# Kernel tuning notes

Hardware: AMD Instinct MI355X
Metric: run time of the kernel (lower is better)

Reference implementation:

```python
import jax, jax.numpy as jnp
import numpy as np

Q = 3  # q_order: SelfONN concatenates powers x^1..x^Q on channel dim

def selfonn_conv(x, w, b, pad):
    # x: (B, C, H, W); w: (O, C*Q, kh, kw); b: (O,)
    xp = jnp.concatenate([x ** (i + 1) for i in range(Q)], axis=1)
    y = jax.lax.conv_general_dilated(
        xp, w, window_strides=(1, 1), padding=[(pad, pad), (pad, pad)],
        dimension_numbers=("NCHW", "OIHW", "NCHW"))
    return y + b[None, :, None, None]

def setup_inputs() -> dict:
    key = jax.random.key(0)
    ks = jax.random.split(key, 9)
    B, C, H, W = 4, 64, 64, 64
    P = 64  # pab_channels
    s1 = 1.0 / np.sqrt(C * Q)          # 1x1 convs
    s3 = 1.0 / np.sqrt(C * Q * 9)      # 3x3 convs
    return {
        "x": jax.random.normal(ks[0], (B, C, H, W), jnp.float32),
        "top_w": jax.random.normal(ks[1], (P, C * Q, 1, 1), jnp.float32) * s1,
        "top_b": jnp.zeros((P,), jnp.float32),
        "center_w": jax.random.normal(ks[2], (P, C * Q, 1, 1), jnp.float32) * s1,
        "center_b": jnp.zeros((P,), jnp.float32),
        "bottom_w": jax.random.normal(ks[3], (C, C * Q, 3, 3), jnp.float32) * s3,
        "bottom_b": jnp.zeros((C,), jnp.float32),
        "out_w": jax.random.normal(ks[4], (C, C * Q, 3, 3), jnp.float32) * s3,
        "out_b": jnp.zeros((C,), jnp.float32),
    }

def reference(x, top_w, top_b, center_w, center_b, bottom_w, bottom_b, out_w, out_b):
    B, C, H, W = x.shape
    HW = H * W
    x_top = selfonn_conv(x, top_w, top_b, 0).reshape(B, -1, HW)            # (B, P, HW)
    x_center = selfonn_conv(x, center_w, center_b, 0).reshape(B, -1, HW)  # (B, P, HW)
    x_bottom = selfonn_conv(x, bottom_w, bottom_b, 1).reshape(B, C, HW)   # (B, C, HW)
    x_center = jnp.swapaxes(x_center, 1, 2)  # (B, HW, P)
    x_bottom = jnp.swapaxes(x_bottom, 1, 2)  # (B, HW, C)
    sp = jnp.einsum("bnp,bpm->bnm", x_center, x_top)  # (B, HW, HW)
    # GLOBAL softmax over the entire HW*HW map per sample (dim=1 on flattened view)
    sp = jax.nn.softmax(sp.reshape(B, -1), axis=1).reshape(B, HW, HW)
    sp = jnp.einsum("bnm,bmc->bnc", sp, x_bottom)  # (B, HW, C)
    # faithful to torch: raw reshape (B, HW, C) -> (B, C, H, W), no transpose
    sp = sp.reshape(B, C, H, W)
    return selfonn_conv(x + sp, out_w, out_b, 1)
```

## Files before the change

kernel.cpp:

```cpp
#include <hip/hip_runtime.h>
#include <hip/hip_bf16.h>

namespace {
constexpr int IMG    = 262144;
constexpr int PADIMG = 4356;
constexpr float LOG2E = 1.44269504088896340736f;
constexpr int WBFO  = 0;
constexpr int XPADO = 122880;
constexpr int TOPO  = 1795584;
constexpr int CENO  = 2319872;
constexpr int BOTO  = 2844160;
constexpr int PVO   = 3368448;
constexpr int MSO4  = 5465600;
constexpr int MSO8  = 7562752;
constexpr size_t NEED8 = (size_t)(MSO8 + 8192) * 4;
}

using half8v  = __attribute__((ext_vector_type(8))) _Float16;
using half4v  = __attribute__((ext_vector_type(4))) _Float16;
using short8v = __attribute__((ext_vector_type(8))) short;
typedef __attribute__((ext_vector_type(4))) float f32x4;

__device__ __forceinline__ short f2bf(float f) {
    __hip_bfloat16 h = __float2bfloat16(f);
    return *reinterpret_cast<short*>(&h);
}
__device__ __forceinline__ float bf2f(short s) {
    unsigned u = ((unsigned)(unsigned short)s) << 16;
    return __uint_as_float(u);
}

__global__ __launch_bounds__(256) void k_prep(const float* __restrict__ bw, const float* __restrict__ ow,
                                              const float* __restrict__ tw, const float* __restrict__ cw,
                                              _Float16* __restrict__ wbf,
                                              const float* __restrict__ x, _Float16* __restrict__ xpad) {
    __shared__ float xs[64 * 65];
    int bx = blockIdx.x, t = threadIdx.x;
    if (bx < 960) {
        int idx = bx * 256 + t;
        if (idx < 221184) {
            int tsel = idx / 110592;
            int r    = idx - tsel * 110592;
            int tap  = r / 12288;
            int rr   = r - tap * 12288;
            int ck   = rr / 2048;
            int r2   = rr - ck * 2048;
            int o    = r2 >> 5;
            int ki   = r2 & 31;
            int k    = ck * 32 + ki;
            int p    = k >> 6, ci = k & 63;
            const float* src = tsel ? ow : bw;
            wbf[idx] = (_Float16)src[o * 1728 + (p * 64 + ci) * 9 + tap];
        } else {
            int j = idx - 221184;
            int tsel = j / 12288;
            int rr   = j - tsel * 12288;
            int ck   = rr / 2048;
            int r2   = rr - ck * 2048;
            int o    = r2 >> 5;
            int ki   = r2 & 31;
            int k    = ck * 32 + ki;
            wbf[idx] = (_Float16)(tsel ? cw[o * 192 + k] * LOG2E : tw[o * 192 + k]);
        }
        return;
    }
    int bx2 = bx - 960;
    int b = bx2 >> 6, h = bx2 & 63;
    {
        _Float16* base = xpad + (size_t)b * 6 * PADIMG * 32;
        int px[6];
        px[0] = (h + 1) * 66;
        px[1] = (h + 1) * 66 + 65;
        px[2] = h;
        px[3] = 65 * 66 + h;
        int npx = 4;
        if (h < 2) { px[4] = 64 + h; px[5] = 65 * 66 + 64 + h; npx = 6; }
        int pi = t / 24, ck = t % 24;
        if (pi < npx) {
            int cp = ck >> 2, q = ck & 3;
            half8v z = {0, 0, 0, 0, 0, 0, 0, 0};
            *(half8v*)&base[((size_t)cp * PADIMG + px[pi]) * 32 + q * 8] = z;
        }
    }
    #pragma unroll
    for (int it = 0; it < 16; ++it) {
        int idx = it * 256 + t;
        int ci = idx >> 6, wc = idx & 63;
        xs[ci * 65 + wc] = x[b * IMG + ci * 4096 + h * 64 + wc];
    }
    __syncthreads();
    _Float16* dst = xpad + ((size_t)b * 6 * PADIMG + (h + 1) * 66 + 1) * 32;
    #pragma unroll
    for (int it = 0; it < 6; ++it) {
        int u = it * 256 + t;
        int ck = u >> 8, within = u & 255;
        int px = within >> 2, q = within & 3;
        int k0 = ck * 32 + q * 8;
        int p = k0 >> 6, c0 = k0 & 63;
        half8v o;
        #pragma unroll
        for (int j = 0; j < 8; ++j) {
            float v = xs[(c0 + j) * 65 + px];
            float pw = (p == 0) ? v : ((p == 1) ? v * v : v * v * v);
            o[j] = (_Float16)pw;
        }
        *(half8v*)&dst[((size_t)ck * PADIMG + px) * 32 + q * 8] = o;
    }
}

__device__ __forceinline__ void conv3d32(int bx, int t,
                                         const _Float16* __restrict__ src,
                                         const _Float16* __restrict__ wt,
                                         const float* __restrict__ bias,
                                         _Float16* __restrict__ dh_, float* __restrict__ df) {
    int lane = t & 63, w = t >> 6;
    int l16 = lane & 15, quad = lane >> 4;
    int oh = bx >> 8, mt = bx & 255;
    int b = mt >> 6, h = mt & 63;
    const _Float16* abase = src + ((size_t)b * 6 * PADIMG + (h + 1) * 66 + 1 + w * 16 + l16) * 32 + quad * 8;
    const _Float16* bbase = wt + (size_t)(oh * 32 + l16) * 32 + quad * 8;
    f32x4 acc[2];
    acc[0] = (f32x4){0.f, 0.f, 0.f, 0.f};
    acc[1] = (f32x4){0.f, 0.f, 0.f, 0.f};
    for (int tap = 0; tap < 9; ++tap) {
        int dh = tap / 3 - 1, dw = tap % 3 - 1;
        const _Float16* arow = abase + (dh * 66 + dw) * 32;
        const _Float16* brow = bbase + (size_t)tap * 6 * 2048;
        #pragma unroll
        for (int c6 = 0; c6 < 6; ++c6) {
            half8v afr  = *(const half8v*)&arow[(size_t)c6 * PADIMG * 32];
            half8v bfr0 = *(const half8v*)&brow[(size_t)c6 * 2048];
            half8v bfr1 = *(const half8v*)&brow[(size_t)c6 * 2048 + 512];
            acc[0] = __builtin_amdgcn_mfma_f32_16x16x32_f16(afr, bfr0, acc[0], 0, 0, 0);
            acc[1] = __builtin_amdgcn_mfma_f32_16x16x32_f16(afr, bfr1, acc[1], 0, 0, 0);
        }
    }
    #pragma unroll
    for (int nf = 0; nf < 2; ++nf) {
        int c = oh * 32 + nf * 16 + l16;
        float bv = bias[c];
        size_t oi = (size_t)b * 262144 + (size_t)c * 4096 + h * 64 + w * 16 + quad * 4;
        if (dh_) {
            half4v o;
            #pragma unroll
            for (int r = 0; r < 4; ++r) o[r] = (_Float16)(acc[nf][r] + bv);
            *(half4v*)&dh_[oi] = o;
        } else {
            float4 o = make_float4(acc[nf][0] + bv, acc[nf][1] + bv, acc[nf][2] + bv, acc[nf][3] + bv);
            *(float4*)&df[oi] = o;
        }
    }
}

__global__ __launch_bounds__(256) void k_convs(const _Float16* __restrict__ xpad,
                                               const _Float16* __restrict__ wbf,
                                               const float* __restrict__ tb, const float* __restrict__ cb,
                                               const float* __restrict__ bbias,
                                               _Float16* __restrict__ topd, _Float16* __restrict__ cend,
                                               _Float16* __restrict__ botb) {
    int bx = blockIdx.x, t = threadIdx.x;
    if (bx < 512) {
        conv3d32(bx, t, xpad, wbf , bbias, botb, nullptr);
        return;
    }
    int bx2 = bx - 512;
    int lane = t & 63, w = t >> 6;
    int l16 = lane & 15, quad = lane >> 4;
    int ot = bx2 >> 8, mt = bx2 & 255;
    int b = mt >> 6, h = mt & 63;
    const _Float16* wt   = wbf + (ot ? 233472 : 221184);
    const float*    bias = ot ? cb : tb;
    _Float16*       dst  = (ot ? cend : topd) + (size_t)b * IMG;
    const _Float16* abase = xpad + ((size_t)b * 6 * PADIMG + (h + 1) * 66 + 1 + w * 16 + l16) * 32 + quad * 8;
    const _Float16* bbase = wt + (size_t)l16 * 32 + quad * 8;
    f32x4 acc[4];
    #pragma unroll
    for (int nf = 0; nf < 4; ++nf) acc[nf] = (f32x4){0.f, 0.f, 0.f, 0.f};
    #pragma unroll
    for (int kc = 0; kc < 6; ++kc) {
        half8v afr = *(const half8v*)&abase[(size_t)kc * PADIMG * 32];
        #pragma unroll
        for (int nf = 0; nf < 4; ++nf) {
            half8v bfr = *(const half8v*)&bbase[(size_t)kc * 2048 + nf * 16 * 32];
            acc[nf] = __builtin_amdgcn_mfma_f32_16x16x32_f16(afr, bfr, acc[nf], 0, 0, 0);
        }
    }
    _Float16* dp = dst + (size_t)(h * 64 + w * 16) * 64;
    #pragma unroll
    for (int nf = 0; nf < 4; ++nf) {
        float bv = bias[nf * 16 + l16];
        if (ot) bv *= LOG2E;
        #pragma unroll
        for (int r = 0; r < 4; ++r)
            dp[(quad * 4 + r) * 64 + nf * 16 + l16] = (_Float16)(acc[nf][r] + bv);
    }
}

__global__ __launch_bounds__(256) void k_attn(float* __restrict__ ws, int mtiles, int msoOff, int zsoOff) {
    __shared__ _Float16 ltop[64 * 72];
    __shared__ _Float16 lbot[64 * 72];
    __shared__ _Float16 lp[128 * 72];
    int t    = threadIdx.x;
    int lane = t & 63, w = t >> 6;
    int l16  = lane & 15, quad = lane >> 4;
    int bxr = blockIdx.x;
    int bx  = (bxr & 7) * ((int)gridDim.x >> 3) + (bxr >> 3);
    int st = bx & 31, b = (bx >> 5) & 3, s = bx >> 7;
    int n0 = st * 128;
    int mbase = s * mtiles * 64;
    const _Float16* topg = (const _Float16*)(ws + TOPO) + (size_t)b * IMG;
    const _Float16* ceng = (const _Float16*)(ws + CENO) + (size_t)b * IMG;
    const _Float16* botg = (const _Float16*)(ws + BOTO) + (size_t)b * IMG;

    half8v afr[2][2];
    #pragma unroll
    for (int i = 0; i < 2; ++i)
        #pragma unroll
        for (int kk = 0; kk < 2; ++kk)
            afr[i][kk] = *(const half8v*)&ceng[(size_t)(n0 + w * 32 + i * 16 + l16) * 64 + kk * 32 + quad * 8];

    int r0 = t >> 3, r1 = r0 + 32, off = (t & 7) * 8;
    int q2 = quad >> 1;
    int lpw = (w * 32 + quad * 4) * 72;
    int lpr = (w * 32 + l16) * 72;
    int rb3 = (l16 >> 3) & 1;

    f32x4 pv[2][4];
    #pragma unroll
    for (int i = 0; i < 2; ++i)
        #pragma unroll
        for (int j = 0; j < 4; ++j) pv[i][j] = (f32x4){0.f, 0.f, 0.f, 0.f};
    float runm = -3.0e38f, zacc = 0.f;

    half8v rt0 = *(const half8v*)&topg[(size_t)(mbase + r0) * 64 + off];
    half8v rt1 = *(const half8v*)&topg[(size_t)(mbase + r1) * 64 + off];
    half8v rb0 = *(const half8v*)&botg[(size_t)r0 * 4096 + mbase + off];
    half8v rb1 = *(const half8v*)&botg[(size_t)r1 * 4096 + mbase + off];

    for (int tt = 0; tt < mtiles; ++tt) {
        __syncthreads();
        *(half8v*)&ltop[r0 * 72 + off] = rt0;
        *(half8v*)&ltop[r1 * 72 + off] = rt1;
        *(half8v*)&lbot[r0 * 72 + off] = rb0;
        *(half8v*)&lbot[r1 * 72 + off] = rb1;
        __syncthreads();
        if (tt < mtiles - 1) {
            int m1 = mbase + (tt + 1) * 64;
            rt0 = *(const half8v*)&topg[(size_t)(m1 + r0) * 64 + off];
            rt1 = *(const half8v*)&topg[(size_t)(m1 + r1) * 64 + off];
            rb0 = *(const half8v*)&botg[(size_t)r0 * 4096 + m1 + off];
            rb1 = *(const half8v*)&botg[(size_t)r1 * 4096 + m1 + off];
        }
        f32x4 sa[2][4];
        #pragma unroll
        for (int i = 0; i < 2; ++i)
            #pragma unroll
            for (int j = 0; j < 4; ++j) sa[i][j] = (f32x4){0.f, 0.f, 0.f, 0.f};
        __builtin_amdgcn_s_setprio(1);
        #pragma unroll
        for (int kk = 0; kk < 2; ++kk)
            #pragma unroll
            for (int j = 0; j < 4; ++j) {
                half8v bfr = *(half8v*)&ltop[(j * 16 + l16) * 72 + kk * 32 + quad * 8];
                sa[0][j] = __builtin_amdgcn_mfma_f32_16x16x32_f16(afr[0][kk], bfr, sa[0][j], 0, 0, 0);
                sa[1][j] = __builtin_amdgcn_mfma_f32_16x16x32_f16(afr[1][kk], bfr, sa[1][j], 0, 0, 0);
            }
        __builtin_amdgcn_s_setprio(0);
        float tm = -3.0e38f;
        #pragma unroll
        for (int i = 0; i < 2; ++i)
            #pragma unroll
            for (int j = 0; j < 4; ++j) {
                float a = fmaxf(sa[i][j][0], sa[i][j][1]);
                float c = fmaxf(sa[i][j][2], sa[i][j][3]);
                tm = fmaxf(tm, fmaxf(a, c));
            }
        for (int o2 = 32; o2; o2 >>= 1) tm = fmaxf(tm, __shfl_xor(tm, o2, 64));
        float newm = fmaxf(runm, tm);
        if (newm > runm) {
            float sc = __builtin_amdgcn_exp2f(runm - newm);
            zacc *= sc;
            #pragma unroll
            for (int i = 0; i < 2; ++i)
                #pragma unroll
                for (int j = 0; j < 4; ++j) pv[i][j] *= sc;
            runm = newm;
        }
        #pragma unroll
        for (int i = 0; i < 2; ++i)
            #pragma unroll
            for (int j = 0; j < 4; ++j) {
                int cb = (j ^ q2) * 16 + l16;
                #pragma unroll
                for (int r = 0; r < 4; ++r) {
                    float e = __builtin_amdgcn_exp2f(sa[i][j][r] - runm);
                    zacc += e;
                    lp[lpw + i * 1152 + r * 72 + cb] = (_Float16)e;
                }
            }
        half8v pa[2][2];
        #pragma unroll
        for (int i = 0; i < 2; ++i)
            #pragma unroll
            for (int kk = 0; kk < 2; ++kk) {
                int jj = kk * 2 + q2;
                pa[i][kk] = *(half8v*)&lp[lpr + i * 1152 + ((jj ^ rb3) * 16) + (quad & 1) * 8];
            }
        __builtin_amdgcn_s_setprio(1);
        #pragma unroll
        for (int kk = 0; kk < 2; ++kk)
            #pragma unroll
            for (int j = 0; j < 4; ++j) {
                half8v bb = *(half8v*)&lbot[(j * 16 + l16) * 72 + kk * 32 + quad * 8];
                pv[0][j] = __builtin_amdgcn_mfma_f32_16x16x32_f16(pa[0][kk], bb, pv[0][j], 0, 0, 0);
                pv[1][j] = __builtin_amdgcn_mfma_f32_16x16x32_f16(pa[1][kk], bb, pv[1][j], 0, 0, 0);
            }
        __builtin_amdgcn_s_setprio(0);
    }
    for (int o2 = 32; o2; o2 >>= 1) zacc += __shfl_xor(zacc, o2, 64);
    if (lane == 0) {
        ws[msoOff + s * 512 + b * 128 + st * 4 + w] = runm;
        ws[zsoOff + s * 512 + b * 128 + st * 4 + w] = zacc;
    }
    short* pvp = (short*)(ws + PVO) + (size_t)s * 1048576 + (size_t)b * IMG;
    #pragma unroll
    for (int i = 0; i < 2; ++i)
        #pragma unroll
        for (int j = 0; j < 4; ++j)
            #pragma unroll
            for (int r = 0; r < 4; ++r)
                pvp[(size_t)(n0 + w * 32 + i * 16 + quad * 4 + r) * 64 + j * 16 + l16] = f2bf(pv[i][j][r]);
}

__global__ __launch_bounds__(512) void k_finalu(const float* __restrict__ x, float* __restrict__ ws,
                                                _Float16* __restrict__ upad,
                                                int ms, int msoOff, int zsoOff) {
    __shared__ float us[64 * 65];
    __shared__ float rm[8], rz[8];
    int t = threadIdx.x, bx = blockIdx.x;
    int b = bx >> 6, h = bx & 63;
    int g = t & 127;
    float m = -3.0e38f;
    for (int s = 0; s < ms; ++s)
        m = fmaxf(m, ws[msoOff + s * 512 + b * 128 + g]);
    for (int o2 = 32; o2; o2 >>= 1) m = fmaxf(m, __shfl_xor(m, o2, 64));
    if ((t & 63) == 0) rm[t >> 6] = m;
    __syncthreads();
    float M = rm[0];
    #pragma unroll
    for (int j = 1; j < 8; ++j) M = fmaxf(M, rm[j]);
    float z = 0.f;
    if (t < 128) {
        for (int s = 0; s < ms; ++s)
            z += ws[zsoOff + s * 512 + b * 128 + g] *
                 __builtin_amdgcn_exp2f(ws[msoOff + s * 512 + b * 128 + g] - M);
    }
    for (int o2 = 32; o2; o2 >>= 1) z += __shfl_xor(z, o2, 64);
    if ((t & 63) == 0) rz[t >> 6] = z;
    __syncthreads();
    float Z = 0.f;
    #pragma unroll
    for (int j = 0; j < 8; ++j) Z += rz[j];
    float rZ = 1.0f / Z;

    const short* pvb = (const short*)(ws + PVO) + (size_t)b * IMG;
    int hg = h >> 5;
    {
        int idx = t * 8;
        int ci = idx >> 6, wc = idx & 63;
        int rem = ci * 4096 + h * 64 + wc;
        int grp = ci * 2 + hg;
        float acc[8] = {};
        for (int s = 0; s < ms; ++s) {
            float scl = __builtin_amdgcn_exp2f(ws[msoOff + s * 512 + b * 128 + grp] - M);
            short8v pvv = *(const short8v*)&pvb[(size_t)s * 1048576 + rem];
            #pragma unroll
            for (int i = 0; i < 8; ++i) acc[i] += bf2f(pvv[i]) * scl;
        }
        float4 x0 = *(const float4*)&x[(size_t)b * IMG + rem];
        float4 x1 = *(const float4*)&x[(size_t)b * IMG + rem + 4];
        float xv[8] = {x0.x, x0.y, x0.z, x0.w, x1.x, x1.y, x1.z, x1.w};
        #pragma unroll
        for (int i = 0; i < 8; ++i)
            us[ci * 65 + wc + i] = xv[i] + acc[i] * rZ;
    }
    __syncthreads();
    _Float16* dst = upad + ((size_t)b * 6 * PADIMG + (h + 1) * 66 + 1) * 32;
    #pragma unroll
    for (int it = 0; it < 3; ++it) {
        int u = it * 512 + t;
        int ck = u >> 8, within = u & 255;
        int px = within >> 2, q = within & 3;
        int k0 = ck * 32 + q * 8;
        int p = k0 >> 6, c0 = k0 & 63;
        half8v o;
        #pragma unroll
        for (int j = 0; j < 8; ++j) {
            float v = us[(c0 + j) * 65 + px];
            float pw = (p == 0) ? v : ((p == 1) ? v * v : v * v * v);
            o[j] = (_Float16)pw;
        }
        *(half8v*)&dst[((size_t)ck * PADIMG + px) * 32 + q * 8] = o;
    }
}

__global__ __launch_bounds__(256) void k_conv3o(const _Float16* __restrict__ upad,
                                                const _Float16* __restrict__ wout,
                                                const float* __restrict__ ob,
                                                float* __restrict__ out) {
    conv3d32(blockIdx.x, threadIdx.x, upad, wout, ob, nullptr, out);
}

extern "C" void kernel_launch(void* const* d_in, const int* in_sizes, int n_in,
                              void* d_out, int out_size, void* d_ws, size_t ws_size,
                              hipStream_t stream) {
    (void)in_sizes; (void)n_in; (void)out_size;
    const float* x  = (const float*)d_in[0];
    const float* tw = (const float*)d_in[1];
    const float* tb = (const float*)d_in[2];
    const float* cw = (const float*)d_in[3];
    const float* cb = (const float*)d_in[4];
    const float* bw = (const float*)d_in[5];
    const float* bb = (const float*)d_in[6];
    const float* ow = (const float*)d_in[7];
    const float* ob = (const float*)d_in[8];
    float* ws  = (float*)d_ws;
    float* out = (float*)d_out;

    _Float16* wbf  = (_Float16*)(ws + WBFO);
    _Float16* wout = wbf + 110592;
    _Float16* xpad = (_Float16*)(ws + XPADO);
    _Float16* topb = (_Float16*)(ws + TOPO);
    _Float16* cenb = (_Float16*)(ws + CENO);
    _Float16* botb = (_Float16*)(ws + BOTO);

    int ms     = (ws_size >= NEED8) ? 8 : 4;
    int mtiles = 64 / ms;
    int msoOff = (ms == 8) ? MSO8 : MSO4;
    int zsoOff = msoOff + ms * 512;

    hipLaunchKernelGGL(k_prep, dim3(1216), dim3(256), 0, stream, bw, ow, tw, cw, wbf, x, xpad);
    hipLaunchKernelGGL(k_convs, dim3(1024), dim3(256), 0, stream, xpad, wbf, tb, cb, bb, topb, cenb, botb);
    hipLaunchKernelGGL(k_attn, dim3(128 * ms), dim3(256), 0, stream, ws, mtiles, msoOff, zsoOff);
    hipLaunchKernelGGL(k_finalu, dim3(256), dim3(512), 0, stream, x, ws, xpad, ms, msoOff, zsoOff);
    hipLaunchKernelGGL(k_conv3o, dim3(512), dim3(256), 0, stream, xpad, wout, ob, out);
}
```

Measured before the change: 168.7 us.

## Keep softmax probabilities in registers via transposed MFMA and lane permutes

Swaps the operand order of the score and PV MFMAs so results come out transposed. The exponentiated probabilities can then be repacked into f16 A/B fragments with cvt_pkrtz, v_permlane32_swap and ds_swizzle instead of a round trip through the LDS buffer. The LDS buffer is removed. Rescaling of the running max is deferred until the local max exceeds it by more than 8, which avoids a per-tile wave reduction. Output stores become 4-wide vectors. The changes add cross-lane permute instructions, and the lazy rescaling lets intermediate values grow up to 2^8, which risks f16 range or precision issues.

New measurement: 167.7 us. No clear change (-0.6%).

```diff
diff --git a/kernel.cpp b/kernel.cpp
--- a/kernel.cpp
+++ b/kernel.cpp
@@ -19,6 +19,8 @@
 using half8v  = __attribute__((ext_vector_type(8))) _Float16;
 using half4v  = __attribute__((ext_vector_type(4))) _Float16;
 using short8v = __attribute__((ext_vector_type(8))) short;
+using short4v = __attribute__((ext_vector_type(4))) short;
+using uint4v  = __attribute__((ext_vector_type(4))) unsigned;
 typedef __attribute__((ext_vector_type(4))) float f32x4;
 
 __device__ __forceinline__ short f2bf(float f) {
@@ -28,6 +30,9 @@
 __device__ __forceinline__ float bf2f(short s) {
     unsigned u = ((unsigned)(unsigned short)s) << 16;
     return __uint_as_float(u);
+}
+__device__ __forceinline__ unsigned pkrtz(float a, float b) {
+    return __builtin_bit_cast(unsigned, __builtin_amdgcn_cvt_pkrtz(a, b));
 }
 
 __global__ __launch_bounds__(256) void k_prep(const float* __restrict__ bw, const float* __restrict__ ow,
@@ -199,10 +204,10 @@
 __global__ __launch_bounds__(256) void k_attn(float* __restrict__ ws, int mtiles, int msoOff, int zsoOff) {
     __shared__ _Float16 ltop[64 * 72];
     __shared__ _Float16 lbot[64 * 72];
-    __shared__ _Float16 lp[128 * 72];
     int t    = threadIdx.x;
     int lane = t & 63, w = t >> 6;
     int l16  = lane & 15, quad = lane >> 4;
+    bool hi16 = (lane & 16) != 0;
     int bxr = blockIdx.x;
     int bx  = (bxr & 7) * ((int)gridDim.x >> 3) + (bxr >> 3);
     int st = bx & 31, b = (bx >> 5) & 3, s = bx >> 7;
@@ -212,24 +217,20 @@
     const _Float16* ceng = (const _Float16*)(ws + CENO) + (size_t)b * IMG;
     const _Float16* botg = (const _Float16*)(ws + BOTO) + (size_t)b * IMG;
 
-    half8v afr[2][2];
-    #pragma unroll
-    for (int i = 0; i < 2; ++i)
+    half8v bcen[2][2];
+    #pragma unroll
+    for (int nj = 0; nj < 2; ++nj)
         #pragma unroll
         for (int kk = 0; kk < 2; ++kk)
-            afr[i][kk] = *(const half8v*)&ceng[(size_t)(n0 + w * 32 + i * 16 + l16) * 64 + kk * 32 + quad * 8];
+            bcen[nj][kk] = *(const half8v*)&ceng[(size_t)(n0 + w * 32 + nj * 16 + l16) * 64 + kk * 32 + quad * 8];
 
     int r0 = t >> 3, r1 = r0 + 32, off = (t & 7) * 8;
-    int q2 = quad >> 1;
-    int lpw = (w * 32 + quad * 4) * 72;
-    int lpr = (w * 32 + l16) * 72;
-    int rb3 = (l16 >> 3) & 1;
-
-    f32x4 pv[2][4];
-    #pragma unroll
-    for (int i = 0; i < 2; ++i)
-        #pragma unroll
-        for (int j = 0; j < 4; ++j) pv[i][j] = (f32x4){0.f, 0.f, 0.f, 0.f};
+
+    f32x4 pv[4][2];
+    #pragma unroll
+    for (int cj = 0; cj < 4; ++cj)
+        #pragma unroll
+        for (int nj = 0; nj < 2; ++nj) pv[cj][nj] = (f32x4){0.f, 0.f, 0.f, 0.f};
     float runm = -3.0e38f, zacc = 0.f;
 
     half8v rt0 = *(const half8v*)&topg[(size_t)(mbase + r0) * 64 + off];
@@ -251,71 +252,85 @@
             rb0 = *(const half8v*)&botg[(size_t)r0 * 4096 + m1 + off];
             rb1 = *(const half8v*)&botg[(size_t)r1 * 4096 + m1 + off];
         }
-        f32x4 sa[2][4];
-        #pragma unroll
-        for (int i = 0; i < 2; ++i)
-            #pragma unroll
-            for (int j = 0; j < 4; ++j) sa[i][j] = (f32x4){0.f, 0.f, 0.f, 0.f};
+        f32x4 sa[4][2];
+        #pragma unroll
+        for (int mi = 0; mi < 4; ++mi)
+            #pragma unroll
+            for (int nj = 0; nj < 2; ++nj) sa[mi][nj] = (f32x4){0.f, 0.f, 0.f, 0.f};
         __builtin_amdgcn_s_setprio(1);
         #pragma unroll
         for (int kk = 0; kk < 2; ++kk)
             #pragma unroll
-            for (int j = 0; j < 4; ++j) {
-                half8v bfr = *(half8v*)&ltop[(j * 16 + l16) * 72 + kk * 32 + quad * 8];
-                sa[0][j] = __builtin_amdgcn_mfma_f32_16x16x32_f16(afr[0][kk], bfr, sa[0][j], 0, 0, 0);
-                sa[1][j] = __builtin_amdgcn_mfma_f32_16x16x32_f16(afr[1][kk], bfr, sa[1][j], 0, 0, 0);
+            for (int mi = 0; mi < 4; ++mi) {
+                half8v at = *(half8v*)&ltop[(mi * 16 + l16) * 72 + kk * 32 + quad * 8];
+                sa[mi][0] = __builtin_amdgcn_mfma_f32_16x16x32_f16(at, bcen[0][kk], sa[mi][0], 0, 0, 0);
+                sa[mi][1] = __builtin_amdgcn_mfma_f32_16x16x32_f16(at, bcen[1][kk], sa[mi][1], 0, 0, 0);
             }
         __builtin_amdgcn_s_setprio(0);
-        float tm = -3.0e38f;
-        #pragma unroll
-        for (int i = 0; i < 2; ++i)
-            #pragma unroll
-            for (int j = 0; j < 4; ++j) {
-                float a = fmaxf(sa[i][j][0], sa[i][j][1]);
-                float c = fmaxf(sa[i][j][2], sa[i][j][3]);
-                tm = fmaxf(tm, fmaxf(a, c));
-            }
-        for (int o2 = 32; o2; o2 >>= 1) tm = fmaxf(tm, __shfl_xor(tm, o2, 64));
-        float newm = fmaxf(runm, tm);
-        if (newm > runm) {
-            float sc = __builtin_amdgcn_exp2f(runm - newm);
-            zacc *= sc;
-            #pragma unroll
-            for (int i = 0; i < 2; ++i)
+        float lm = -3.0e38f;
+        #pragma unroll
+        for (int mi = 0; mi < 4; ++mi)
+            #pragma unroll
+            for (int nj = 0; nj < 2; ++nj) {
+                float a = fmaxf(sa[mi][nj][0], sa[mi][nj][1]);
+                float c2 = fmaxf(sa[mi][nj][2], sa[mi][nj][3]);
+                lm = fmaxf(lm, fmaxf(a, c2));
+            }
+        if (!__all(lm - runm <= 8.0f)) {
+            float tm = lm;
+            for (int o2 = 32; o2; o2 >>= 1) tm = fmaxf(tm, __shfl_xor(tm, o2, 64));
+            if (tm > runm) {
+                float sc = __builtin_amdgcn_exp2f(runm - tm);
+                zacc *= sc;
                 #pragma unroll
-                for (int j = 0; j < 4; ++j) pv[i][j] *= sc;
-            runm = newm;
-        }
-        #pragma unroll
-        for (int i = 0; i < 2; ++i)
-            #pragma unroll
-            for (int j = 0; j < 4; ++j) {
-                int cb = (j ^ q2) * 16 + l16;
+                for (int cj = 0; cj < 4; ++cj)
+                    #pragma unroll
+                    for (int nj = 0; nj < 2; ++nj) pv[cj][nj] *= sc;
+                runm = tm;
+            }
+        }
+        #pragma unroll
+        for (int kb = 0; kb < 2; ++kb) {
+            unsigned pk[2][2][2];
+            #pragma unroll
+            for (int f = 0; f < 2; ++f) {
+                int mi = 2 * kb + f;
                 #pragma unroll
-                for (int r = 0; r < 4; ++r) {
-                    float e = __builtin_amdgcn_exp2f(sa[i][j][r] - runm);
-                    zacc += e;
-                    lp[lpw + i * 1152 + r * 72 + cb] = (_Float16)e;
+                for (int nj = 0; nj < 2; ++nj) {
+                    float e0 = __builtin_amdgcn_exp2f(sa[mi][nj][0] - runm);
+                    float e1 = __builtin_amdgcn_exp2f(sa[mi][nj][1] - runm);
+                    float e2 = __builtin_amdgcn_exp2f(sa[mi][nj][2] - runm);
+                    float e3 = __builtin_amdgcn_exp2f(sa[mi][nj][3] - runm);
+                    zacc += (e0 + e1) + (e2 + e3);
+                    pk[f][nj][0] = pkrtz(e0, e1);
+                    pk[f][nj][1] = pkrtz(e2, e3);
                 }
             }
-        half8v pa[2][2];
-        #pragma unroll
-        for (int i = 0; i < 2; ++i)
-            #pragma unroll
-            for (int kk = 0; kk < 2; ++kk) {
-                int jj = kk * 2 + q2;
-                pa[i][kk] = *(half8v*)&lp[lpr + i * 1152 + ((jj ^ rb3) * 16) + (quad & 1) * 8];
-            }
-        __builtin_amdgcn_s_setprio(1);
-        #pragma unroll
-        for (int kk = 0; kk < 2; ++kk)
-            #pragma unroll
-            for (int j = 0; j < 4; ++j) {
-                half8v bb = *(half8v*)&lbot[(j * 16 + l16) * 72 + kk * 32 + quad * 8];
-                pv[0][j] = __builtin_amdgcn_mfma_f32_16x16x32_f16(pa[0][kk], bb, pv[0][j], 0, 0, 0);
-                pv[1][j] = __builtin_amdgcn_mfma_f32_16x16x32_f16(pa[1][kk], bb, pv[1][j], 0, 0, 0);
-            }
-        __builtin_amdgcn_s_setprio(0);
+            half8v pa[2];
+            #pragma unroll
+            for (int nj = 0; nj < 2; ++nj) {
+                unsigned T[4];
+                #pragma unroll
+                for (int d = 0; d < 2; ++d) {
+                    unsigned X = pk[0][nj][d], Y = pk[1][nj][d];
+                    asm("v_permlane32_swap_b32 %0, %1" : "+v"(X), "+v"(Y));
+                    unsigned A0s = __builtin_amdgcn_ds_swizzle(X, 0x401F);
+                    unsigned A1s = __builtin_amdgcn_ds_swizzle(Y, 0x401F);
+                    T[d]     = hi16 ? A1s : X;
+                    T[d + 2] = hi16 ? Y : A0s;
+                }
+                uint4v tv = {T[0], T[1], T[2], T[3]};
+                pa[nj] = __builtin_bit_cast(half8v, tv);
+            }
+            __builtin_amdgcn_s_setprio(1);
+            #pragma unroll
+            for (int cj = 0; cj < 4; ++cj) {
+                half8v ab = *(half8v*)&lbot[(cj * 16 + l16) * 72 + kb * 32 + quad * 8];
+                pv[cj][0] = __builtin_amdgcn_mfma_f32_16x16x32_f16(ab, pa[0], pv[cj][0], 0, 0, 0);
+                pv[cj][1] = __builtin_amdgcn_mfma_f32_16x16x32_f16(ab, pa[1], pv[cj][1], 0, 0, 0);
+            }
+            __builtin_amdgcn_s_setprio(0);
+        }
     }
     for (int o2 = 32; o2; o2 >>= 1) zacc += __shfl_xor(zacc, o2, 64);
     if (lane == 0) {
@@ -324,12 +339,14 @@
     }
     short* pvp = (short*)(ws + PVO) + (size_t)s * 1048576 + (size_t)b * IMG;
     #pragma unroll
-    for (int i = 0; i < 2; ++i)
-        #pragma unroll
-        for (int j = 0; j < 4; ++j)
-            #pragma unroll
-            for (int r = 0; r < 4; ++r)
-                pvp[(size_t)(n0 + w * 32 + i * 16 + quad * 4 + r) * 64 + j * 16 + l16] = f2bf(pv[i][j][r]);
+    for (int cj = 0; cj < 4; ++cj)
+        #pragma unroll
+        for (int nj = 0; nj < 2; ++nj) {
+            short4v o;
+            #pragma unroll
+            for (int r = 0; r < 4; ++r) o[r] = f2bf(pv[cj][nj][r]);
+            *(short4v*)&pvp[(size_t)(n0 + w * 32 + nj * 16 + l16) * 64 + cj * 16 + quad * 4] = o;
+        }
 }
 
 __global__ __launch_bounds__(512) void k_finalu(const float* __restrict__ x, float* __restrict__ ws,
```
